# Kernel tuning notes

Measured on AMD Instinct MI355X. Metric: run time of the kernel, lower is better.

Reference implementation:

```python
import jax, jax.numpy as jnp
import numpy as np

B, C, D, H = 4, 1024, 768, 12      # batch, seq_len(>512 long-doc), hidden, heads
E, K, S, V, P = 32, 2, 24, 8, 512  # entities, mentions/entity, sents, virtual nodes, ht pairs
NT = 256                            # node type embedding dim
EMB, BLK, NL = 768, 64, 97          # emb_size, block_size, num_labels
OFFSET = 1


def setup_inputs() -> dict:
    key = jax.random.key(0)
    ks = jax.random.split(key, 13)
    return {
        "sequence_output": jax.random.normal(ks[0], (B, C, D), jnp.float32),
        "attention": jax.random.uniform(ks[1], (B, H, C, C), jnp.float32),
        "entity_pos": jax.random.randint(ks[2], (B, E, K), 0, C - 2),
        "sent_pos": jax.random.randint(ks[3], (B, S), 0, C - 2),
        "virtual_pos": jax.random.randint(ks[4], (B, V), 0, C - 2),
        "hts": jax.random.randint(ks[5], (B, P, 2), 0, E),
        "node_type_emb": jax.random.normal(ks[6], (B, E, NT), jnp.float32) * 0.02,
        "W_head": jax.random.normal(ks[7], (2 * D + NT, EMB), jnp.float32) * 0.02,
        "b_head": jnp.zeros((EMB,), jnp.float32),
        "W_tail": jax.random.normal(ks[8], (2 * D + NT, EMB), jnp.float32) * 0.02,
        "b_tail": jnp.zeros((EMB,), jnp.float32),
        "W_bil": jax.random.normal(ks[9], (EMB * BLK, NL), jnp.float32) * 0.02,
        "b_bil": jnp.zeros((NL,), jnp.float32),
    }


def reference(sequence_output, attention, entity_pos, sent_pos, virtual_pos, hts,
              node_type_emb, W_head, b_head, W_tail, b_tail, W_bil, b_bil):
    # --- get_mention_embed / get_entity_embed: gather mention-start rows ---
    idx = entity_pos + OFFSET                      # [B,E,K] token index of each mention start
    flat = idx.reshape(B, E * K)                   # mention order matches torch double loop
    mention_embed = jnp.take_along_axis(sequence_output, flat[:, :, None], axis=1)  # [B,E*K,D]
    entity_embed = jax.nn.logsumexp(mention_embed.reshape(B, E, K, D), axis=2)      # [B,E,D]

    # --- get_sent_embed / get_virtual_embed: single-row gathers ---
    sent_embed = jnp.take_along_axis(sequence_output, (sent_pos + OFFSET)[:, :, None], axis=1)      # [B,S,D]
    virtual_embed = jnp.take_along_axis(sequence_output, (virtual_pos + OFFSET)[:, :, None], axis=1)  # [B,V,D]

    # --- get_rss: localized-context pooling over attention ---
    att_t = attention.transpose(0, 2, 1, 3)        # [B,C,H,C] so we gather query rows
    e_att = jnp.take_along_axis(att_t, flat[:, :, None, None], axis=1)  # [B,E*K,H,C]
    e_att = e_att.reshape(B, E, K, H, C).mean(axis=2)                   # [B,E,H,C] mean over mentions
    h_att = jnp.take_along_axis(e_att, hts[:, :, 0][:, :, None, None], axis=1)  # [B,P,H,C]
    t_att = jnp.take_along_axis(e_att, hts[:, :, 1][:, :, None, None], axis=1)  # [B,P,H,C]
    ht_att = (h_att * t_att).mean(axis=2)                               # [B,P,C] mean over heads
    ht_att = ht_att / (ht_att.sum(axis=-1, keepdims=True) + 1e-5)
    rs = jnp.einsum('bld,brl->brd', sequence_output, ht_att)            # [B,P,D]

    # --- get_pair_entity_embed on entity hidden state (entity_embed + node-type emb) ---
    ent_hidden = jnp.concatenate([entity_embed, node_type_emb], axis=-1)          # [B,E,D+NT]
    s_emb = jnp.take_along_axis(ent_hidden, hts[:, :, 0][:, :, None], axis=1)     # [B,P,D+NT]
    t_emb = jnp.take_along_axis(ent_hidden, hts[:, :, 1][:, :, None], axis=1)

    # --- head/tail extractors + grouped bilinear classifier ---
    hs = jnp.tanh(jnp.concatenate([s_emb, rs], axis=-1) @ W_head + b_head)  # [B,P,EMB]
    ts = jnp.tanh(jnp.concatenate([t_emb, rs], axis=-1) @ W_tail + b_tail)
    b1 = hs.reshape(B, P, EMB // BLK, BLK)
    b2 = ts.reshape(B, P, EMB // BLK, BLK)
    bl = (b1[..., :, None] * b2[..., None, :]).reshape(B, P, EMB * BLK)     # [B,P,EMB*BLK]
    logits = bl @ W_bil + b_bil                                             # [B,P,NL]
    return (logits, mention_embed, sent_embed, virtual_embed)
```

## Files before the change

kernel.cpp:

```cpp
#include <hip/hip_runtime.h>

#define B_   4
#define C_   1024
#define D_   768
#define H_   12
#define E_   32
#define K_   2
#define S_   24
#define V_   8
#define P_   512
#define NT_  256
#define EMB_ 768
#define BLK_ 64
#define NL_  97
#define DNT_ 1024
#define KHT_ 1792
#define KBIL_ 49152
#define NPAD_ 128

typedef __bf16 bf16x8 __attribute__((ext_vector_type(8)));
typedef float  f32x4  __attribute__((ext_vector_type(4)));

__device__ __forceinline__ float b2f(unsigned short u) {
    return (float)__builtin_bit_cast(__bf16, u);
}
__device__ __forceinline__ unsigned short f2b(float f) {
    return __builtin_bit_cast(unsigned short, (__bf16)f);
}
__device__ __forceinline__ float ld_in(const void* p, size_t i, int isf) {
    return isf ? ((const float*)p)[i] : b2f(((const unsigned short*)p)[i]);
}
__device__ __forceinline__ void st_out(void* p, size_t i, float v, int isf) {
    if (isf) ((float*)p)[i] = v;
    else     ((unsigned short*)p)[i] = f2b(v);
}
__device__ __forceinline__ int probe_isf(const void* seq) {
    unsigned short u = ((const unsigned short*)seq)[2 * (threadIdx.x & 63)];
    int huge = !(fabsf(b2f(u)) <= 1e10f);
    unsigned long long zb = __ballot(u == 0);
    return __any(huge) || (__popcll(zb) > 56);
}

#define PREP_GATHER 256
#define PREP_EATT   (PREP_GATHER + B_*E_*H_)
#define PREP_TSEQ   (PREP_EATT + 768)
#define PREP_TW     (PREP_TSEQ + 672)
#define PREP_TBIL   (PREP_TW + 768)

__global__ __launch_bounds__(256) void k_prep(
    const void* __restrict__ seq, const void* __restrict__ att,
    const int* __restrict__ epos, const int* __restrict__ spos,
    const int* __restrict__ vpos, const void* __restrict__ ntype,
    const void* __restrict__ Wh, const void* __restrict__ Wt_,
    const void* __restrict__ Wb,
    float* __restrict__ enth, unsigned short* __restrict__ e_att,
    unsigned short* __restrict__ seqT,
    unsigned short* __restrict__ WtH, unsigned short* __restrict__ WtT,
    unsigned short* __restrict__ WtB,
    void* __restrict__ outv, long long moff, long long soff, long long voff)
{
    __shared__ __align__(16) unsigned char smem[12544];
    int blk = blockIdx.x, tid = threadIdx.x;
    int isf = probe_isf(seq);
    if (blk < PREP_GATHER) {
        if (blk < B_ * E_) {
            int b = blk / E_, e = blk % E_;
            int i0 = epos[(b * E_ + e) * K_ + 0] + 1;
            int i1 = epos[(b * E_ + e) * K_ + 1] + 1;
            size_t r0 = ((size_t)b * C_ + i0) * D_;
            size_t r1 = ((size_t)b * C_ + i1) * D_;
            size_t m0 = (size_t)moff + ((size_t)(b * E_ * K_) + 2 * e) * D_;
            size_t m1 = m0 + D_;
            float* eh = enth + (size_t)(b * E_ + e) * DNT_;
            for (int d = tid; d < D_; d += 256) {
                float a = ld_in(seq, r0 + d, isf);
                float c = ld_in(seq, r1 + d, isf);
                st_out(outv, m0 + d, a, isf);
                st_out(outv, m1 + d, c, isf);
                float mx = fmaxf(a, c);
                eh[d] = mx + logf(expf(a - mx) + expf(c - mx));
            }
            size_t nt0 = (size_t)(b * E_ + e) * NT_;
            for (int j = tid; j < NT_; j += 256) eh[D_ + j] = ld_in(ntype, nt0 + j, isf);
        } else if (blk < B_ * E_ + B_ * S_) {
            int t = blk - B_ * E_; int b = t / S_, s = t % S_;
            int i = spos[b * S_ + s] + 1;
            size_t r = ((size_t)b * C_ + i) * D_;
            size_t o = (size_t)soff + (size_t)(b * S_ + s) * D_;
            for (int d = tid; d < D_; d += 256) st_out(outv, o + d, ld_in(seq, r + d, isf), isf);
        } else {
            int t = blk - B_ * E_ - B_ * S_; int b = t / V_, v = t % V_;
            int i = vpos[b * V_ + v] + 1;
            size_t r = ((size_t)b * C_ + i) * D_;
            size_t o = (size_t)voff + (size_t)(b * V_ + v) * D_;
            for (int d = tid; d < D_; d += 256) st_out(outv, o + d, ld_in(seq, r + d, isf), isf);
        }
    } else if (blk < PREP_EATT) {
        int t = blk - PREP_GATHER;
        int b = t / (E_ * H_); int r = t % (E_ * H_); int e = r / H_; int h = r % H_;
        int i0 = epos[(b * E_ + e) * K_ + 0] + 1;
        int i1 = epos[(b * E_ + e) * K_ + 1] + 1;
        size_t a0 = (((size_t)b * H_ + h) * C_ + i0) * C_;
        size_t a1 = (((size_t)b * H_ + h) * C_ + i1) * C_;
        unsigned short* o = e_att + (((size_t)(b * E_ + e)) * H_ + h) * C_;
        for (int c = tid; c < C_; c += 256)
            o[c] = f2b(0.5f * (ld_in(att, a0 + c, isf) + ld_in(att, a1 + c, isf)));
    } else if (blk < PREP_TSEQ) {
        int t = blk - PREP_EATT;
        int b = t / 192; int r = t % 192; int ct = r / 12; int dt = r % 12;
        typedef unsigned short row65[65];
        row65* tile = (row65*)smem;
        for (int idx = tid; idx < 4096; idx += 256) {
            int cc = idx >> 6, dd = idx & 63;
            tile[cc][dd] = f2b(ld_in(seq, ((size_t)b * C_ + ct * 64 + cc) * D_ + dt * 64 + dd, isf));
        }
        __syncthreads();
        for (int idx = tid; idx < 4096; idx += 256) {
            int dd = idx >> 6, cc = idx & 63;
            seqT[((size_t)b * D_ + dt * 64 + dd) * C_ + ct * 64 + cc] = tile[cc][dd];
        }
    } else if (blk < PREP_TW) {
        int t = blk - PREP_TSEQ;
        int mat = t / 336; int r = t % 336; int kt = r / 12; int nt = r % 12;
        const void* in = mat ? Wt_ : Wh;
        unsigned short* out = mat ? WtT : WtH;
        typedef unsigned short row65[65];
        row65* tile = (row65*)smem;
        for (int idx = tid; idx < 4096; idx += 256) {
            int kk = idx >> 6, nn = idx & 63;
            tile[kk][nn] = f2b(ld_in(in, ((size_t)kt * 64 + kk) * EMB_ + nt * 64 + nn, isf));
        }
        __syncthreads();
        for (int idx = tid; idx < 4096; idx += 256) {
            int nn = idx >> 6, kk = idx & 63;
            out[((size_t)nt * 64 + nn) * KHT_ + kt * 64 + kk] = tile[kk][nn];
        }
    } else {
        int t = blk - PREP_TW;
        int k0 = t << 6;
        unsigned short* raw = (unsigned short*)smem;
        for (int idx = tid; idx < 64 * NL_; idx += 256)
            raw[idx] = f2b(ld_in(Wb, (size_t)k0 * NL_ + idx, isf));
        __syncthreads();
        int kk = tid & 63, nq = tid >> 6;
        for (int i = 0; i < 32; i++) {
            int n = nq * 32 + i;
            unsigned short v = (n < NL_) ? raw[kk * NL_ + n] : (unsigned short)0;
            WtB[(size_t)n * KBIL_ + k0 + kk] = v;
        }
    }
}

__global__ __launch_bounds__(256) void k_mid(
    const unsigned short* __restrict__ e_att, const float* __restrict__ enth,
    const int* __restrict__ hts,
    unsigned short* __restrict__ htb,
    unsigned short* __restrict__ Xh, unsigned short* __restrict__ Xt,
    float* __restrict__ logitsF)
{
    __shared__ float red[4];
    int blk = blockIdx.x, tid = threadIdx.x;
    if (blk < B_ * P_) {
        int b = blk >> 9;
        int he = hts[blk * 2 + 0], te = hts[blk * 2 + 1];
        const unsigned short* ph = e_att + (size_t)(b * E_ + he) * H_ * C_;
        const unsigned short* pt = e_att + (size_t)(b * E_ + te) * H_ * C_;
        float v[4]; float ls = 0.f;
        for (int ci = 0; ci < 4; ci++) {
            int c = tid + (ci << 8);
            float acc = 0.f;
#pragma unroll
            for (int h = 0; h < H_; h++) acc += b2f(ph[h * C_ + c]) * b2f(pt[h * C_ + c]);
            acc *= (1.0f / (float)H_);
            v[ci] = acc; ls += acc;
        }
        for (int off = 32; off > 0; off >>= 1) ls += __shfl_down(ls, off, 64);
        if ((tid & 63) == 0) red[tid >> 6] = ls;
        __syncthreads();
        float inv = 1.0f / (red[0] + red[1] + red[2] + red[3] + 1e-5f);
        for (int ci = 0; ci < 4; ci++)
            htb[((size_t)blk << 10) + tid + (ci << 8)] = f2b(v[ci] * inv);
    } else if (blk < 2 * B_ * P_) {
        int m = blk - B_ * P_; int b = m >> 9;
        int eh = hts[m * 2 + 0], et = hts[m * 2 + 1];
        const float* sh = enth + (size_t)(b * E_ + eh) * DNT_;
        const float* st = enth + (size_t)(b * E_ + et) * DNT_;
        for (int k = tid; k < DNT_; k += 256) {
            Xh[(size_t)m * KHT_ + k] = f2b(sh[k]);
            Xt[(size_t)m * KHT_ + k] = f2b(st[k]);
        }
    } else {
        int t = blk - 2 * B_ * P_;
        ((float4*)logitsF)[(size_t)t * 256 + tid] = make_float4(0.f, 0.f, 0.f, 0.f);
    }
}

__global__ __launch_bounds__(256) void k_gemm(
    const unsigned short* __restrict__ A0, const unsigned short* __restrict__ A1,
    const unsigned short* __restrict__ B0, const unsigned short* __restrict__ B1,
    long long lda, long long ldb, long long sAz, long long sBz,
    int nsteps, int zmode,
    const void* __restrict__ bias0, const void* __restrict__ bias1,
    unsigned short* __restrict__ oY0, unsigned short* __restrict__ oY1,
    unsigned short* __restrict__ oX1, unsigned short* __restrict__ oX2,
    const void* __restrict__ seq)
{
    int n0 = blockIdx.x * 64, m0 = blockIdx.y * 64, z = blockIdx.z;
    const unsigned short* Ab; const unsigned short* Bb;
    unsigned short* oY = nullptr; const void* bias = nullptr;
    if (zmode == 0) {
        Ab = A0 + (size_t)z * sAz; Bb = B0 + (size_t)z * sBz;
    } else {
        Ab = z ? A1 : A0; Bb = z ? B1 : B0;
        oY = z ? oY1 : oY0; bias = z ? bias1 : bias0;
    }
    __shared__ __align__(16) unsigned short a_lds[64][40];
    __shared__ __align__(16) unsigned short b_lds[64][40];
    int tid = threadIdx.x, lane = tid & 63, w = tid >> 6;
    int wm = (w >> 1) * 32, wn = (w & 1) * 32, q = lane >> 4, l15 = lane & 15;
    f32x4 acc00 = {0.f,0.f,0.f,0.f}, acc01 = acc00, acc10 = acc00, acc11 = acc00;
    int srow = tid >> 2, sch = (tid & 3) * 8;
    const unsigned short* pa = Ab + (size_t)(m0 + srow) * lda + sch;
    const unsigned short* pb = Bb + (size_t)(n0 + srow) * ldb + sch;
    int4 ra = *(const int4*)pa;
    int4 rb = *(const int4*)pb;
    for (int ks = 0; ks < nsteps; ks++) {
        __syncthreads();
        *(int4*)&a_lds[srow][sch] = ra;
        *(int4*)&b_lds[srow][sch] = rb;
        __syncthreads();
        if (ks + 1 < nsteps) {
            ra = *(const int4*)(pa + (size_t)(ks + 1) * 32);
            rb = *(const int4*)(pb + (size_t)(ks + 1) * 32);
        }
        bf16x8 a0 = *(const bf16x8*)&a_lds[wm + l15][q * 8];
        bf16x8 a1 = *(const bf16x8*)&a_lds[wm + 16 + l15][q * 8];
        bf16x8 b0 = *(const bf16x8*)&b_lds[wn + l15][q * 8];
        bf16x8 b1 = *(const bf16x8*)&b_lds[wn + 16 + l15][q * 8];
        acc00 = __builtin_amdgcn_mfma_f32_16x16x32_bf16(a0, b0, acc00, 0, 0, 0);
        acc01 = __builtin_amdgcn_mfma_f32_16x16x32_bf16(a0, b1, acc01, 0, 0, 0);
        acc10 = __builtin_amdgcn_mfma_f32_16x16x32_bf16(a1, b0, acc10, 0, 0, 0);
        acc11 = __builtin_amdgcn_mfma_f32_16x16x32_bf16(a1, b1, acc11, 0, 0, 0);
    }
    f32x4 accs[2][2] = {{acc00, acc01}, {acc10, acc11}};
    int isf = (zmode == 1) ? probe_isf(seq) : 0;
#pragma unroll
    for (int mt = 0; mt < 2; mt++)
#pragma unroll
        for (int nt = 0; nt < 2; nt++) {
            int gmb = m0 + wm + mt * 16 + q * 4;
            int gn  = n0 + wn + nt * 16 + l15;
            if (zmode == 0) {
#pragma unroll
                for (int r = 0; r < 4; r++) {
                    unsigned short v = f2b(accs[mt][nt][r]);
                    size_t o = (size_t)(z * P_ + gmb + r) * KHT_ + DNT_ + gn;
                    oX1[o] = v; oX2[o] = v;
                }
            } else {
                float bv = ld_in(bias, gn, isf);
#pragma unroll
                for (int r = 0; r < 4; r++)
                    oY[(size_t)(gmb + r) * EMB_ + gn] = f2b(tanhf(accs[mt][nt][r] + bv));
            }
        }
}

__global__ __launch_bounds__(256) void k_bil(
    const unsigned short* __restrict__ hsB, const unsigned short* __restrict__ tsB,
    const unsigned short* __restrict__ WtB, float* __restrict__ logitsF)
{
    int m0 = blockIdx.x * 32;
    int g  = blockIdx.y;
    int tid = threadIdx.x, lane = tid & 63, w = tid >> 6;
    int q = lane >> 4, l15 = lane & 15;
    __shared__ __align__(16) unsigned short hsl[32][80];
    __shared__ __align__(16) unsigned short tsl[32][80];
    for (int idx = tid; idx < 512; idx += 256) {
        int m = idx >> 4, j4 = (idx & 15) * 4;
        *(ushort4*)&hsl[m][j4] = *(const ushort4*)&hsB[(size_t)(m0 + m) * EMB_ + g * 64 + j4];
        *(ushort4*)&tsl[m][j4] = *(const ushort4*)&tsB[(size_t)(m0 + m) * EMB_ + g * 64 + j4];
    }
    __syncthreads();

    const unsigned short* pB0 = WtB + (size_t)(w * 16 + l15) * KBIL_ + g * 4096 + q * 8;
    const unsigned short* pB1 = pB0 + (size_t)64 * KBIL_;
    bf16x8 rb0[2], rb1[2];
    rb0[0] = *(const bf16x8*)(pB0);      rb1[0] = *(const bf16x8*)(pB1);
    rb0[1] = *(const bf16x8*)(pB0 + 32); rb1[1] = *(const bf16x8*)(pB1 + 32);
    f32x4 acc00 = {0.f,0.f,0.f,0.f}, acc01 = acc00, acc10 = acc00, acc11 = acc00;

#pragma unroll 2
    for (int kk = 0; kk < 128; kk++) {
        int sl = kk & 1;
        bf16x8 bw0 = rb0[sl], bw1 = rb1[sl];
        if (kk + 2 < 128) {
            rb0[sl] = *(const bf16x8*)(pB0 + (size_t)(kk + 2) * 32);
            rb1[sl] = *(const bf16x8*)(pB1 + (size_t)(kk + 2) * 32);
        }
        int i = kk >> 1, h = kk & 1;
        float ha0 = b2f(hsl[l15][i]);
        float ha1 = b2f(hsl[16 + l15][i]);
        bf16x8 t0 = *(const bf16x8*)&tsl[l15][h * 32 + q * 8];
        bf16x8 t1 = *(const bf16x8*)&tsl[16 + l15][h * 32 + q * 8];
        bf16x8 af0, af1;
#pragma unroll
        for (int j = 0; j < 8; j++) {
            af0[j] = (__bf16)(ha0 * (float)t0[j]);
            af1[j] = (__bf16)(ha1 * (float)t1[j]);
        }
        acc00 = __builtin_amdgcn_mfma_f32_16x16x32_bf16(af0, bw0, acc00, 0, 0, 0);
        acc01 = __builtin_amdgcn_mfma_f32_16x16x32_bf16(af0, bw1, acc01, 0, 0, 0);
        acc10 = __builtin_amdgcn_mfma_f32_16x16x32_bf16(af1, bw0, acc10, 0, 0, 0);
        acc11 = __builtin_amdgcn_mfma_f32_16x16x32_bf16(af1, bw1, acc11, 0, 0, 0);
    }
#pragma unroll
    for (int r = 0; r < 4; r++) {
        atomicAdd(&logitsF[(size_t)(m0 + q * 4 + r) * NPAD_ + w * 16 + l15],           acc00[r]);
        atomicAdd(&logitsF[(size_t)(m0 + q * 4 + r) * NPAD_ + w * 16 + 64 + l15],      acc01[r]);
        atomicAdd(&logitsF[(size_t)(m0 + 16 + q * 4 + r) * NPAD_ + w * 16 + l15],      acc10[r]);
        atomicAdd(&logitsF[(size_t)(m0 + 16 + q * 4 + r) * NPAD_ + w * 16 + 64 + l15], acc11[r]);
    }
}

__global__ __launch_bounds__(256) void k_fin(
    const float* __restrict__ logitsF, const void* __restrict__ b_bil,
    void* __restrict__ outv, const void* __restrict__ seq)
{
    int isf = probe_isf(seq);
    int idx = blockIdx.x * 256 + threadIdx.x;
    if (idx >= B_ * P_ * NL_) return;
    int m = idx / NL_, n = idx % NL_;
    st_out(outv, idx, logitsF[(size_t)m * NPAD_ + n] + ld_in(b_bil, n, isf), isf);
}

extern "C" void kernel_launch(void* const* d_in, const int* in_sizes, int n_in,
                              void* d_out, int out_size, void* d_ws, size_t ws_size,
                              hipStream_t stream)
{
    const void* seq    = d_in[0];
    const void* att    = d_in[1];
    const int*  epos   = (const int*)d_in[2];
    const int*  spos   = (const int*)d_in[3];
    const int*  vpos   = (const int*)d_in[4];
    const int*  hts    = (const int*)d_in[5];
    const void* ntype  = d_in[6];
    const void* W_head = d_in[7];
    const void* b_head = d_in[8];
    const void* W_tail = d_in[9];
    const void* b_tail = d_in[10];
    const void* W_bil  = d_in[11];
    const void* b_bil  = d_in[12];

    long long mention_off = (long long)B_ * P_ * NL_;
    long long sent_off    = mention_off + (long long)B_ * E_ * K_ * D_;
    long long virt_off    = sent_off + (long long)B_ * S_ * D_;

    char* p = (char*)d_ws;
    auto alloc = [&](size_t bytes) { void* r = (void*)p; p += (bytes + 255) & ~(size_t)255; return r; };
    unsigned short* e_att   = (unsigned short*)alloc((size_t)B_ * E_ * H_ * C_ * 2);
    unsigned short* htb     = (unsigned short*)alloc((size_t)B_ * P_ * C_ * 2);
    unsigned short* seqT    = (unsigned short*)alloc((size_t)B_ * D_ * C_ * 2);
    unsigned short* WtH     = (unsigned short*)alloc((size_t)EMB_ * KHT_ * 2);
    unsigned short* WtT     = (unsigned short*)alloc((size_t)EMB_ * KHT_ * 2);
    unsigned short* WtB     = (unsigned short*)alloc((size_t)NPAD_ * KBIL_ * 2);
    unsigned short* Xh      = (unsigned short*)alloc((size_t)B_ * P_ * KHT_ * 2);
    unsigned short* Xt      = (unsigned short*)alloc((size_t)B_ * P_ * KHT_ * 2);
    unsigned short* hsB     = (unsigned short*)alloc((size_t)B_ * P_ * EMB_ * 2);
    unsigned short* tsB     = (unsigned short*)alloc((size_t)B_ * P_ * EMB_ * 2);
    float*          logitsF = (float*)alloc((size_t)B_ * P_ * NPAD_ * 4);
    float*          enth    = (float*)alloc((size_t)B_ * E_ * DNT_ * 4);

    dim3 blk(256);
    k_prep<<<PREP_TBIL, blk, 0, stream>>>(
        seq, att, epos, spos, vpos, ntype, W_head, W_tail, W_bil,
        enth, e_att, seqT, WtH, WtT, WtB,
        d_out, mention_off, sent_off, virt_off);
    k_mid<<<2 * B_ * P_ + 256, blk, 0, stream>>>(e_att, enth, hts, htb, Xh, Xt, logitsF);
    k_gemm<<<dim3(EMB_ / 64, P_ / 64, B_), blk, 0, stream>>>(
        htb, nullptr, seqT, nullptr, C_, C_,
        (long long)P_ * C_, (long long)D_ * C_, C_ / 32, 0,
        nullptr, nullptr, nullptr, nullptr, Xh, Xt, seq);
    k_gemm<<<dim3(EMB_ / 64, (B_ * P_) / 64, 2), blk, 0, stream>>>(
        Xh, Xt, WtH, WtT, KHT_, KHT_, 0, 0, KHT_ / 32, 1,
        b_head, b_tail, hsB, tsB, nullptr, nullptr, seq);
    k_bil<<<dim3((B_ * P_) / 32, 12, 1), blk, 0, stream>>>(hsB, tsB, WtB, logitsF);
    k_fin<<<(B_ * P_ * NL_ + 255) / 256, blk, 0, stream>>>(logitsF, b_bil, d_out, seq);
}
```

Baseline: 447.5 us.

## Factor bilinear classifier: MFMA over tail block, scale by head scalar in fp32

The grouped bilinear kernel no longer forms the hs⊗ts outer-product operand in bf16 at each K step. For each head index i it runs MFMAs of the tail block against the matching W_bil slice, then scales the partial sums by the head value in fp32 and accumulates. The tile grows to 64 rows with 512-thread blocks, and the block index is remapped so blocks sharing a weight slice are scheduled together. This removes the per-step bf16 conversion work and doubles reuse of each weight load. The cost is twice as many MFMAs per useful product (the K=64 reduction is split into two K=32 MFMAs starting from zero) and a transposed LDS store of hs that may cause bank conflicts.

```diff
diff --git a/kernel.cpp b/kernel.cpp
--- a/kernel.cpp
+++ b/kernel.cpp
@@ -266,60 +266,89 @@
         }
 }
 
-__global__ __launch_bounds__(256) void k_bil(
+__global__ __launch_bounds__(512) void k_bil(
     const unsigned short* __restrict__ hsB, const unsigned short* __restrict__ tsB,
     const unsigned short* __restrict__ WtB, float* __restrict__ logitsF)
 {
-    int m0 = blockIdx.x * 32;
-    int g  = blockIdx.y;
+    int bid = blockIdx.x;
+    int lin = (bid & 7) * 48 + (bid >> 3);
+    int g   = lin >> 5;
+    int m0  = (lin & 31) * 64;
+
     int tid = threadIdx.x, lane = tid & 63, w = tid >> 6;
     int q = lane >> 4, l15 = lane & 15;
-    __shared__ __align__(16) unsigned short hsl[32][80];
-    __shared__ __align__(16) unsigned short tsl[32][80];
-    for (int idx = tid; idx < 512; idx += 256) {
-        int m = idx >> 4, j4 = (idx & 15) * 4;
-        *(ushort4*)&hsl[m][j4] = *(const ushort4*)&hsB[(size_t)(m0 + m) * EMB_ + g * 64 + j4];
-        *(ushort4*)&tsl[m][j4] = *(const ushort4*)&tsB[(size_t)(m0 + m) * EMB_ + g * 64 + j4];
+    int wm = (w >> 2) * 32;
+    int wn = (w & 3) * 16;
+
+    __shared__ __align__(16) unsigned short tsl[64][72];
+    __shared__ __align__(16) unsigned short hsT[64][64];
+    {
+        int m = tid >> 3, j0 = (tid & 7) * 8;
+        const unsigned short* ph = &hsB[(size_t)(m0 + m) * EMB_ + g * 64 + j0];
+        const unsigned short* pt = &tsB[(size_t)(m0 + m) * EMB_ + g * 64 + j0];
+        ushort4 h0 = *(const ushort4*)ph, h1 = *(const ushort4*)(ph + 4);
+        ushort4 t0 = *(const ushort4*)pt, t1 = *(const ushort4*)(pt + 4);
+        *(ushort4*)&tsl[m][j0]     = t0;
+        *(ushort4*)&tsl[m][j0 + 4] = t1;
+        hsT[j0+0][m] = h0.x; hsT[j0+1][m] = h0.y; hsT[j0+2][m] = h0.z; hsT[j0+3][m] = h0.w;
+        hsT[j0+4][m] = h1.x; hsT[j0+5][m] = h1.y; hsT[j0+6][m] = h1.z; hsT[j0+7][m] = h1.w;
     }
     __syncthreads();
 
-    const unsigned short* pB0 = WtB + (size_t)(w * 16 + l15) * KBIL_ + g * 4096 + q * 8;
-    const unsigned short* pB1 = pB0 + (size_t)64 * KBIL_;
-    bf16x8 rb0[2], rb1[2];
-    rb0[0] = *(const bf16x8*)(pB0);      rb1[0] = *(const bf16x8*)(pB1);
-    rb0[1] = *(const bf16x8*)(pB0 + 32); rb1[1] = *(const bf16x8*)(pB1 + 32);
+    bf16x8 a00 = *(const bf16x8*)&tsl[wm + l15][q * 8];
+    bf16x8 a01 = *(const bf16x8*)&tsl[wm + l15][32 + q * 8];
+    bf16x8 a10 = *(const bf16x8*)&tsl[wm + 16 + l15][q * 8];
+    bf16x8 a11 = *(const bf16x8*)&tsl[wm + 16 + l15][32 + q * 8];
+
+    const unsigned short* pW0 = WtB + (size_t)(wn + l15) * KBIL_ + g * 4096 + q * 8;
+    const unsigned short* pW1 = pW0 + (size_t)64 * KBIL_;
+
     f32x4 acc00 = {0.f,0.f,0.f,0.f}, acc01 = acc00, acc10 = acc00, acc11 = acc00;
-
-#pragma unroll 2
-    for (int kk = 0; kk < 128; kk++) {
-        int sl = kk & 1;
-        bf16x8 bw0 = rb0[sl], bw1 = rb1[sl];
-        if (kk + 2 < 128) {
-            rb0[sl] = *(const bf16x8*)(pB0 + (size_t)(kk + 2) * 32);
-            rb1[sl] = *(const bf16x8*)(pB1 + (size_t)(kk + 2) * 32);
-        }
-        int i = kk >> 1, h = kk & 1;
-        float ha0 = b2f(hsl[l15][i]);
-        float ha1 = b2f(hsl[16 + l15][i]);
-        bf16x8 t0 = *(const bf16x8*)&tsl[l15][h * 32 + q * 8];
-        bf16x8 t1 = *(const bf16x8*)&tsl[16 + l15][h * 32 + q * 8];
-        bf16x8 af0, af1;
-#pragma unroll
-        for (int j = 0; j < 8; j++) {
-            af0[j] = (__bf16)(ha0 * (float)t0[j]);
-            af1[j] = (__bf16)(ha1 * (float)t1[j]);
-        }
-        acc00 = __builtin_amdgcn_mfma_f32_16x16x32_bf16(af0, bw0, acc00, 0, 0, 0);
-        acc01 = __builtin_amdgcn_mfma_f32_16x16x32_bf16(af0, bw1, acc01, 0, 0, 0);
-        acc10 = __builtin_amdgcn_mfma_f32_16x16x32_bf16(af1, bw0, acc10, 0, 0, 0);
-        acc11 = __builtin_amdgcn_mfma_f32_16x16x32_bf16(af1, bw1, acc11, 0, 0, 0);
-    }
-#pragma unroll
-    for (int r = 0; r < 4; r++) {
-        atomicAdd(&logitsF[(size_t)(m0 + q * 4 + r) * NPAD_ + w * 16 + l15],           acc00[r]);
-        atomicAdd(&logitsF[(size_t)(m0 + q * 4 + r) * NPAD_ + w * 16 + 64 + l15],      acc01[r]);
-        atomicAdd(&logitsF[(size_t)(m0 + 16 + q * 4 + r) * NPAD_ + w * 16 + l15],      acc10[r]);
-        atomicAdd(&logitsF[(size_t)(m0 + 16 + q * 4 + r) * NPAD_ + w * 16 + 64 + l15], acc11[r]);
+    const f32x4 zf = {0.f,0.f,0.f,0.f};
+
+    bf16x8 wc0 = *(const bf16x8*)(pW0);
+    bf16x8 wc1 = *(const bf16x8*)(pW0 + 32);
+    bf16x8 wc2 = *(const bf16x8*)(pW1);
+    bf16x8 wc3 = *(const bf16x8*)(pW1 + 32);
+    bf16x8 wx0 = wc0, wx1 = wc1, wx2 = wc2, wx3 = wc3;
+
+    for (int i = 0; i < 64; ++i) {
+        if (i + 1 < 64) {
+            const unsigned short* q0 = pW0 + (size_t)(i + 1) * 64;
+            const unsigned short* q1 = pW1 + (size_t)(i + 1) * 64;
+            wx0 = *(const bf16x8*)(q0); wx1 = *(const bf16x8*)(q0 + 32);
+            wx2 = *(const bf16x8*)(q1); wx3 = *(const bf16x8*)(q1 + 32);
+        }
+        f32x4 p00 = __builtin_amdgcn_mfma_f32_16x16x32_bf16(a00, wc0, zf, 0, 0, 0);
+        p00       = __builtin_amdgcn_mfma_f32_16x16x32_bf16(a01, wc1, p00, 0, 0, 0);
+        f32x4 p01 = __builtin_amdgcn_mfma_f32_16x16x32_bf16(a00, wc2, zf, 0, 0, 0);
+        p01       = __builtin_amdgcn_mfma_f32_16x16x32_bf16(a01, wc3, p01, 0, 0, 0);
+        f32x4 p10 = __builtin_amdgcn_mfma_f32_16x16x32_bf16(a10, wc0, zf, 0, 0, 0);
+        p10       = __builtin_amdgcn_mfma_f32_16x16x32_bf16(a11, wc1, p10, 0, 0, 0);
+        f32x4 p11 = __builtin_amdgcn_mfma_f32_16x16x32_bf16(a10, wc2, zf, 0, 0, 0);
+        p11       = __builtin_amdgcn_mfma_f32_16x16x32_bf16(a11, wc3, p11, 0, 0, 0);
+
+        ushort4 hv0 = *(const ushort4*)&hsT[i][wm + q * 4];
+        ushort4 hv1 = *(const ushort4*)&hsT[i][wm + 16 + q * 4];
+        float ha00 = b2f(hv0.x), ha01 = b2f(hv0.y), ha02 = b2f(hv0.z), ha03 = b2f(hv0.w);
+        float ha10 = b2f(hv1.x), ha11 = b2f(hv1.y), ha12 = b2f(hv1.z), ha13 = b2f(hv1.w);
+        acc00[0] += ha00 * p00[0]; acc00[1] += ha01 * p00[1];
+        acc00[2] += ha02 * p00[2]; acc00[3] += ha03 * p00[3];
+        acc01[0] += ha00 * p01[0]; acc01[1] += ha01 * p01[1];
+        acc01[2] += ha02 * p01[2]; acc01[3] += ha03 * p01[3];
+        acc10[0] += ha10 * p10[0]; acc10[1] += ha11 * p10[1];
+        acc10[2] += ha12 * p10[2]; acc10[3] += ha13 * p10[3];
+        acc11[0] += ha10 * p11[0]; acc11[1] += ha11 * p11[1];
+        acc11[2] += ha12 * p11[2]; acc11[3] += ha13 * p11[3];
+
+        wc0 = wx0; wc1 = wx1; wc2 = wx2; wc3 = wx3;
+    }
+#pragma unroll
+    for (int r = 0; r < 4; ++r) {
+        atomicAdd(&logitsF[(size_t)(m0 + wm + q * 4 + r) * NPAD_ + wn + l15],           acc00[r]);
+        atomicAdd(&logitsF[(size_t)(m0 + wm + q * 4 + r) * NPAD_ + wn + 64 + l15],      acc01[r]);
+        atomicAdd(&logitsF[(size_t)(m0 + wm + 16 + q * 4 + r) * NPAD_ + wn + l15],      acc10[r]);
+        atomicAdd(&logitsF[(size_t)(m0 + wm + 16 + q * 4 + r) * NPAD_ + wn + 64 + l15], acc11[r]);
     }
 }
 
@@ -384,6 +413,6 @@
     k_gemm<<<dim3(EMB_ / 64, (B_ * P_) / 64, 2), blk, 0, stream>>>(
         Xh, Xt, WtH, WtT, KHT_, KHT_, 0, 0, KHT_ / 32, 1,
         b_head, b_tail, hsB, tsB, nullptr, nullptr, seq);
-    k_bil<<<dim3((B_ * P_) / 32, 12, 1), blk, 0, stream>>>(hsB, tsB, WtB, logitsF);
+    k_bil<<<dim3((B_ * P_ / 64) * 12), dim3(512), 0, stream>>>(hsB, tsB, WtB, logitsF);
     k_fin<<<(B_ * P_ * NL_ + 255) / 256, blk, 0, stream>>>(logitsF, b_bil, d_out, seq);
 }
```

Result: slower. 464.4 us (+3.8%).

## Restructure bilinear classifier as per-head-element MFMA with LDS-staged weights

Applied to the files above, without the earlier changes.

The grouped bilinear kernel now computes, for each head element i, the product of the tail block with the matching weight slice on the MFMA units, then scales by the head value in fp32 and accumulates. This replaces building the outer-product A operand in registers with bf16 rounding. Weight slices are streamed into LDS with async global-to-LDS loads, using double buffering and an XOR swizzle. Tiles grow to 128 rows with 512 threads, the K dimension is split four ways per group, and blocks are remapped for locality. The trade-off is more MFMA work per useful FLOP, since each K=64 product runs per i, plus atomics across the four K-splits.

```diff
diff --git a/kernel.cpp b/kernel.cpp
--- a/kernel.cpp
+++ b/kernel.cpp
@@ -266,61 +266,133 @@
         }
 }
 
-__global__ __launch_bounds__(256) void k_bil(
+__global__ __launch_bounds__(512, 4) void k_bil(
     const unsigned short* __restrict__ hsB, const unsigned short* __restrict__ tsB,
     const unsigned short* __restrict__ WtB, float* __restrict__ logitsF)
 {
-    int m0 = blockIdx.x * 32;
-    int g  = blockIdx.y;
+    int bid = blockIdx.x;
+    int lin = (bid & 7) * 96 + (bid >> 3);
+    int mt  = lin & 15;
+    int gic = lin >> 4;
+    int g   = gic >> 2;
+    int ic  = gic & 3;
+    int m0  = mt * 128;
+
     int tid = threadIdx.x, lane = tid & 63, w = tid >> 6;
     int q = lane >> 4, l15 = lane & 15;
-    __shared__ __align__(16) unsigned short hsl[32][80];
-    __shared__ __align__(16) unsigned short tsl[32][80];
-    for (int idx = tid; idx < 512; idx += 256) {
-        int m = idx >> 4, j4 = (idx & 15) * 4;
-        *(ushort4*)&hsl[m][j4] = *(const ushort4*)&hsB[(size_t)(m0 + m) * EMB_ + g * 64 + j4];
-        *(ushort4*)&tsl[m][j4] = *(const ushort4*)&tsB[(size_t)(m0 + m) * EMB_ + g * 64 + j4];
-    }
+    int mg = (w >> 2) * 64;
+    int ng = (w & 3) * 32;
+
+    __shared__ __align__(16) unsigned short wbuf[2][8192];
+    __shared__ __align__(16) unsigned short hsT[16][128];
+
+    if (tid < 128) {
+        const unsigned short* ph = &hsB[(size_t)(m0 + tid) * EMB_ + g * 64 + ic * 16];
+        ushort4 h0 = *(const ushort4*)(ph + 0);
+        ushort4 h1 = *(const ushort4*)(ph + 4);
+        ushort4 h2 = *(const ushort4*)(ph + 8);
+        ushort4 h3 = *(const ushort4*)(ph + 12);
+        hsT[ 0][tid] = h0.x; hsT[ 1][tid] = h0.y; hsT[ 2][tid] = h0.z; hsT[ 3][tid] = h0.w;
+        hsT[ 4][tid] = h1.x; hsT[ 5][tid] = h1.y; hsT[ 6][tid] = h1.z; hsT[ 7][tid] = h1.w;
+        hsT[ 8][tid] = h2.x; hsT[ 9][tid] = h2.y; hsT[10][tid] = h2.z; hsT[11][tid] = h2.w;
+        hsT[12][tid] = h3.x; hsT[13][tid] = h3.y; hsT[14][tid] = h3.z; hsT[15][tid] = h3.w;
+    }
+
+    bf16x8 a[4][2];
+#pragma unroll
+    for (int ms = 0; ms < 4; ++ms)
+#pragma unroll
+        for (int jh = 0; jh < 2; ++jh)
+            a[ms][jh] = *(const bf16x8*)&tsB[(size_t)(m0 + mg + ms * 16 + l15) * EMB_
+                                             + g * 64 + jh * 32 + q * 8];
+
     __syncthreads();
 
-    const unsigned short* pB0 = WtB + (size_t)(w * 16 + l15) * KBIL_ + g * 4096 + q * 8;
-    const unsigned short* pB1 = pB0 + (size_t)64 * KBIL_;
-    bf16x8 rb0[2], rb1[2];
-    rb0[0] = *(const bf16x8*)(pB0);      rb1[0] = *(const bf16x8*)(pB1);
-    rb0[1] = *(const bf16x8*)(pB0 + 32); rb1[1] = *(const bf16x8*)(pB1 + 32);
-    f32x4 acc00 = {0.f,0.f,0.f,0.f}, acc01 = acc00, acc10 = acc00, acc11 = acc00;
-
-#pragma unroll 2
-    for (int kk = 0; kk < 128; kk++) {
-        int sl = kk & 1;
-        bf16x8 bw0 = rb0[sl], bw1 = rb1[sl];
-        if (kk + 2 < 128) {
-            rb0[sl] = *(const bf16x8*)(pB0 + (size_t)(kk + 2) * 32);
-            rb1[sl] = *(const bf16x8*)(pB1 + (size_t)(kk + 2) * 32);
-        }
-        int i = kk >> 1, h = kk & 1;
-        float ha0 = b2f(hsl[l15][i]);
-        float ha1 = b2f(hsl[16 + l15][i]);
-        bf16x8 t0 = *(const bf16x8*)&tsl[l15][h * 32 + q * 8];
-        bf16x8 t1 = *(const bf16x8*)&tsl[16 + l15][h * 32 + q * 8];
-        bf16x8 af0, af1;
-#pragma unroll
-        for (int j = 0; j < 8; j++) {
-            af0[j] = (__bf16)(ha0 * (float)t0[j]);
-            af1[j] = (__bf16)(ha1 * (float)t1[j]);
-        }
-        acc00 = __builtin_amdgcn_mfma_f32_16x16x32_bf16(af0, bw0, acc00, 0, 0, 0);
-        acc01 = __builtin_amdgcn_mfma_f32_16x16x32_bf16(af0, bw1, acc01, 0, 0, 0);
-        acc10 = __builtin_amdgcn_mfma_f32_16x16x32_bf16(af1, bw0, acc10, 0, 0, 0);
-        acc11 = __builtin_amdgcn_mfma_f32_16x16x32_bf16(af1, bw1, acc11, 0, 0, 0);
-    }
-#pragma unroll
-    for (int r = 0; r < 4; r++) {
-        atomicAdd(&logitsF[(size_t)(m0 + q * 4 + r) * NPAD_ + w * 16 + l15],           acc00[r]);
-        atomicAdd(&logitsF[(size_t)(m0 + q * 4 + r) * NPAD_ + w * 16 + 64 + l15],      acc01[r]);
-        atomicAdd(&logitsF[(size_t)(m0 + 16 + q * 4 + r) * NPAD_ + w * 16 + l15],      acc10[r]);
-        atomicAdd(&logitsF[(size_t)(m0 + 16 + q * 4 + r) * NPAD_ + w * 16 + 64 + l15], acc11[r]);
-    }
+    size_t gbase = (size_t)g * 4096 + (size_t)ic * 16 * 64;
+    int flat0 = tid, flat1 = 512 + tid;
+    int n0r = flat0 >> 3, n1r = flat1 >> 3;
+    const unsigned short* src0 = WtB + (size_t)n0r * KBIL_ + gbase + ((flat0 & 7) ^ (n0r & 7)) * 8;
+    const unsigned short* src1 = WtB + (size_t)n1r * KBIL_ + gbase + ((flat1 & 7) ^ (n1r & 7)) * 8;
+    unsigned short* dst0 = &wbuf[0][0] + (size_t)(0 * 512 + w * 64) * 8;
+    unsigned short* dst1 = &wbuf[0][0] + (size_t)(1 * 512 + w * 64) * 8;
+
+#define STAGE_W(islice, buf)                                                              \
+    do {                                                                                  \
+        size_t joff = (size_t)(islice) * 64;                                              \
+        __builtin_amdgcn_global_load_lds(                                                 \
+            (const __attribute__((address_space(1))) void*)(src0 + joff),                 \
+            (__attribute__((address_space(3))) void*)(dst0 + (size_t)(buf) * 8192), 16, 0, 0); \
+        __builtin_amdgcn_global_load_lds(                                                 \
+            (const __attribute__((address_space(1))) void*)(src1 + joff),                 \
+            (__attribute__((address_space(3))) void*)(dst1 + (size_t)(buf) * 8192), 16, 0, 0); \
+    } while (0)
+
+    STAGE_W(0, 0);
+    STAGE_W(1, 1);
+    asm volatile("s_waitcnt vmcnt(2)" ::: "memory");
+    __builtin_amdgcn_s_barrier();
+
+    f32x4 acc[4][2];
+#pragma unroll
+    for (int ms = 0; ms < 4; ++ms)
+#pragma unroll
+        for (int nt = 0; nt < 2; ++nt)
+            acc[ms][nt] = (f32x4){0.f, 0.f, 0.f, 0.f};
+    const f32x4 zf = {0.f, 0.f, 0.f, 0.f};
+
+    for (int i = 0; i < 16; ++i) {
+        int cur = i & 1;
+        const char* wb = (const char*)&wbuf[cur][0];
+        bf16x8 wf[2][2];
+#pragma unroll
+        for (int nt = 0; nt < 2; ++nt) {
+            int nrow = ng + nt * 16 + l15;
+            int sw = (nrow & 7) << 4;
+#pragma unroll
+            for (int jh = 0; jh < 2; ++jh)
+                wf[nt][jh] = *(const bf16x8*)(wb + ((nrow * 128 + jh * 64 + q * 16) ^ sw));
+        }
+        f32x4 p[4][2];
+#pragma unroll
+        for (int ms = 0; ms < 4; ++ms)
+#pragma unroll
+            for (int nt = 0; nt < 2; ++nt) {
+                f32x4 t = __builtin_amdgcn_mfma_f32_16x16x32_bf16(a[ms][0], wf[nt][0], zf, 0, 0, 0);
+                p[ms][nt] = __builtin_amdgcn_mfma_f32_16x16x32_bf16(a[ms][1], wf[nt][1], t, 0, 0, 0);
+            }
+#pragma unroll
+        for (int ms = 0; ms < 4; ++ms) {
+            ushort4 hv = *(const ushort4*)&hsT[i][mg + ms * 16 + q * 4];
+            float h0 = b2f(hv.x), h1 = b2f(hv.y), h2 = b2f(hv.z), h3 = b2f(hv.w);
+#pragma unroll
+            for (int nt = 0; nt < 2; ++nt) {
+                acc[ms][nt][0] += h0 * p[ms][nt][0];
+                acc[ms][nt][1] += h1 * p[ms][nt][1];
+                acc[ms][nt][2] += h2 * p[ms][nt][2];
+                acc[ms][nt][3] += h3 * p[ms][nt][3];
+            }
+        }
+        asm volatile("" ::: "memory");
+        __builtin_amdgcn_s_barrier();
+        if (i + 2 < 16) {
+            STAGE_W(i + 2, cur);
+            asm volatile("s_waitcnt vmcnt(2)" ::: "memory");
+        } else {
+            asm volatile("s_waitcnt vmcnt(0)" ::: "memory");
+        }
+        __builtin_amdgcn_s_barrier();
+    }
+#undef STAGE_W
+
+#pragma unroll
+    for (int ms = 0; ms < 4; ++ms)
+#pragma unroll
+        for (int nt = 0; nt < 2; ++nt)
+#pragma unroll
+            for (int r = 0; r < 4; ++r)
+                atomicAdd(&logitsF[(size_t)(m0 + mg + ms * 16 + q * 4 + r) * NPAD_
+                                   + ng + nt * 16 + l15],
+                          acc[ms][nt][r]);
 }
 
 __global__ __launch_bounds__(256) void k_fin(
@@ -384,6 +456,6 @@
     k_gemm<<<dim3(EMB_ / 64, (B_ * P_) / 64, 2), blk, 0, stream>>>(
         Xh, Xt, WtH, WtT, KHT_, KHT_, 0, 0, KHT_ / 32, 1,
         b_head, b_tail, hsB, tsB, nullptr, nullptr, seq);
-    k_bil<<<dim3((B_ * P_) / 32, 12, 1), blk, 0, stream>>>(hsB, tsB, WtB, logitsF);
+    k_bil<<<dim3(16 * 12 * 4), dim3(512), 0, stream>>>(hsB, tsB, WtB, logitsF);
     k_fin<<<(B_ * P_ * NL_ + 255) / 256, blk, 0, stream>>>(logitsF, b_bil, d_out, seq);
 }
```

Result: slower. 759.1 us (+69.6%).

## Factor bilinear product: MFMA ts·W per i, then scale by hs in fp32

Applied to the files above, without the earlier changes.

Restructures the grouped bilinear kernel. It computes ts × W_bil blocks with MFMA using tsB fragments held in registers, then multiplies each partial by the hs scalar in fp32. Before, the hs×ts outer-product operand was rebuilt in bf16 every step. The kernel now uses 512-thread blocks covering 64 rows, all 128 padded labels and half a group, with a swizzled block index meant to improve weight reuse in L2. This does twice as many MFMAs per accumulated result and adds fp32 FMAs, but it drops the per-step conversion work and changes rounding.

```diff
diff --git a/kernel.cpp b/kernel.cpp
--- a/kernel.cpp
+++ b/kernel.cpp
@@ -266,61 +266,86 @@
         }
 }
 
-__global__ __launch_bounds__(256) void k_bil(
+__global__ __launch_bounds__(512) void k_bil(
     const unsigned short* __restrict__ hsB, const unsigned short* __restrict__ tsB,
     const unsigned short* __restrict__ WtB, float* __restrict__ logitsF)
 {
-    int m0 = blockIdx.x * 32;
-    int g  = blockIdx.y;
+    int bid = blockIdx.x;
+    int lin = (bid & 7) * 96 + (bid >> 3);
+    int mt  = lin & 31;
+    int gic = lin >> 5;
+    int g   = gic >> 1;
+    int ic  = gic & 1;
+    int m0  = mt * 64;
+
     int tid = threadIdx.x, lane = tid & 63, w = tid >> 6;
     int q = lane >> 4, l15 = lane & 15;
-    __shared__ __align__(16) unsigned short hsl[32][80];
-    __shared__ __align__(16) unsigned short tsl[32][80];
-    for (int idx = tid; idx < 512; idx += 256) {
-        int m = idx >> 4, j4 = (idx & 15) * 4;
-        *(ushort4*)&hsl[m][j4] = *(const ushort4*)&hsB[(size_t)(m0 + m) * EMB_ + g * 64 + j4];
-        *(ushort4*)&tsl[m][j4] = *(const ushort4*)&tsB[(size_t)(m0 + m) * EMB_ + g * 64 + j4];
-    }
+    int ns = w * 16;
+
+    __shared__ __align__(16) unsigned short hsT[32][64];
+    {
+        int m = tid >> 3, i4 = (tid & 7) * 4;
+        ushort4 hv = *(const ushort4*)&hsB[(size_t)(m0 + m) * EMB_ + g * 64 + ic * 32 + i4];
+        hsT[i4 + 0][m] = hv.x; hsT[i4 + 1][m] = hv.y;
+        hsT[i4 + 2][m] = hv.z; hsT[i4 + 3][m] = hv.w;
+    }
+
+    bf16x8 a[4][2];
+#pragma unroll
+    for (int ms = 0; ms < 4; ++ms)
+#pragma unroll
+        for (int jh = 0; jh < 2; ++jh)
+            a[ms][jh] = *(const bf16x8*)&tsB[(size_t)(m0 + ms * 16 + l15) * EMB_
+                                             + g * 64 + jh * 32 + q * 8];
     __syncthreads();
 
-    const unsigned short* pB0 = WtB + (size_t)(w * 16 + l15) * KBIL_ + g * 4096 + q * 8;
-    const unsigned short* pB1 = pB0 + (size_t)64 * KBIL_;
-    bf16x8 rb0[2], rb1[2];
-    rb0[0] = *(const bf16x8*)(pB0);      rb1[0] = *(const bf16x8*)(pB1);
-    rb0[1] = *(const bf16x8*)(pB0 + 32); rb1[1] = *(const bf16x8*)(pB1 + 32);
-    f32x4 acc00 = {0.f,0.f,0.f,0.f}, acc01 = acc00, acc10 = acc00, acc11 = acc00;
-
-#pragma unroll 2
-    for (int kk = 0; kk < 128; kk++) {
-        int sl = kk & 1;
-        bf16x8 bw0 = rb0[sl], bw1 = rb1[sl];
-        if (kk + 2 < 128) {
-            rb0[sl] = *(const bf16x8*)(pB0 + (size_t)(kk + 2) * 32);
-            rb1[sl] = *(const bf16x8*)(pB1 + (size_t)(kk + 2) * 32);
-        }
-        int i = kk >> 1, h = kk & 1;
-        float ha0 = b2f(hsl[l15][i]);
-        float ha1 = b2f(hsl[16 + l15][i]);
-        bf16x8 t0 = *(const bf16x8*)&tsl[l15][h * 32 + q * 8];
-        bf16x8 t1 = *(const bf16x8*)&tsl[16 + l15][h * 32 + q * 8];
-        bf16x8 af0, af1;
-#pragma unroll
-        for (int j = 0; j < 8; j++) {
-            af0[j] = (__bf16)(ha0 * (float)t0[j]);
-            af1[j] = (__bf16)(ha1 * (float)t1[j]);
-        }
-        acc00 = __builtin_amdgcn_mfma_f32_16x16x32_bf16(af0, bw0, acc00, 0, 0, 0);
-        acc01 = __builtin_amdgcn_mfma_f32_16x16x32_bf16(af0, bw1, acc01, 0, 0, 0);
-        acc10 = __builtin_amdgcn_mfma_f32_16x16x32_bf16(af1, bw0, acc10, 0, 0, 0);
-        acc11 = __builtin_amdgcn_mfma_f32_16x16x32_bf16(af1, bw1, acc11, 0, 0, 0);
-    }
-#pragma unroll
-    for (int r = 0; r < 4; r++) {
-        atomicAdd(&logitsF[(size_t)(m0 + q * 4 + r) * NPAD_ + w * 16 + l15],           acc00[r]);
-        atomicAdd(&logitsF[(size_t)(m0 + q * 4 + r) * NPAD_ + w * 16 + 64 + l15],      acc01[r]);
-        atomicAdd(&logitsF[(size_t)(m0 + 16 + q * 4 + r) * NPAD_ + w * 16 + l15],      acc10[r]);
-        atomicAdd(&logitsF[(size_t)(m0 + 16 + q * 4 + r) * NPAD_ + w * 16 + 64 + l15], acc11[r]);
-    }
+    const unsigned short* pw = WtB + (size_t)(ns + l15) * KBIL_ + g * 4096 + ic * 2048 + q * 8;
+
+    f32x4 acc[4];
+#pragma unroll
+    for (int ms = 0; ms < 4; ++ms) acc[ms] = (f32x4){0.f, 0.f, 0.f, 0.f};
+    const f32x4 zf = {0.f, 0.f, 0.f, 0.f};
+
+    bf16x8 w0a = *(const bf16x8*)(pw);
+    bf16x8 w0b = *(const bf16x8*)(pw + 32);
+    bf16x8 w1a = *(const bf16x8*)(pw + 64);
+    bf16x8 w1b = *(const bf16x8*)(pw + 96);
+
+#define BIL_STEP(ii, wa_, wb_)                                                             \
+    do {                                                                                   \
+        int ipre = (ii) + 2 <= 31 ? (ii) + 2 : 31;                                         \
+        bf16x8 na = *(const bf16x8*)(pw + (size_t)ipre * 64);                              \
+        bf16x8 nb = *(const bf16x8*)(pw + (size_t)ipre * 64 + 32);                         \
+        f32x4 p[4];                                                                        \
+        _Pragma("unroll")                                                                  \
+        for (int ms = 0; ms < 4; ++ms) {                                                   \
+            f32x4 t = __builtin_amdgcn_mfma_f32_16x16x32_bf16(a[ms][0], wa_, zf, 0, 0, 0); \
+            p[ms]   = __builtin_amdgcn_mfma_f32_16x16x32_bf16(a[ms][1], wb_, t, 0, 0, 0);  \
+        }                                                                                  \
+        _Pragma("unroll")                                                                  \
+        for (int ms = 0; ms < 4; ++ms) {                                                   \
+            ushort4 hv = *(const ushort4*)&hsT[ii][ms * 16 + q * 4];                       \
+            acc[ms][0] += b2f(hv.x) * p[ms][0];                                            \
+            acc[ms][1] += b2f(hv.y) * p[ms][1];                                            \
+            acc[ms][2] += b2f(hv.z) * p[ms][2];                                            \
+            acc[ms][3] += b2f(hv.w) * p[ms][3];                                            \
+        }                                                                                  \
+        wa_ = na; wb_ = nb;                                                                \
+    } while (0)
+
+#pragma unroll 4
+    for (int ii = 0; ii < 16; ++ii) {
+        BIL_STEP(2 * ii,     w0a, w0b);
+        BIL_STEP(2 * ii + 1, w1a, w1b);
+    }
+#undef BIL_STEP
+
+#pragma unroll
+    for (int ms = 0; ms < 4; ++ms)
+#pragma unroll
+        for (int r = 0; r < 4; ++r)
+            atomicAdd(&logitsF[(size_t)(m0 + ms * 16 + q * 4 + r) * NPAD_ + ns + l15],
+                      acc[ms][r]);
 }
 
 __global__ __launch_bounds__(256) void k_fin(
@@ -384,6 +409,6 @@
     k_gemm<<<dim3(EMB_ / 64, (B_ * P_) / 64, 2), blk, 0, stream>>>(
         Xh, Xt, WtH, WtT, KHT_, KHT_, 0, 0, KHT_ / 32, 1,
         b_head, b_tail, hsB, tsB, nullptr, nullptr, seq);
-    k_bil<<<dim3((B_ * P_) / 32, 12, 1), blk, 0, stream>>>(hsB, tsB, WtB, logitsF);
+    k_bil<<<dim3(768), dim3(512), 0, stream>>>(hsB, tsB, WtB, logitsF);
     k_fin<<<(B_ * P_ * NL_ + 255) / 256, blk, 0, stream>>>(logitsF, b_bil, d_out, seq);
 }
```

After: 412.8 us. 1.08x faster.
